# Performance work log

Measured on AMD Instinct MI355X. Metric: run time of the kernel, lower is better.

## Reference

```python
import jax, jax.numpy as jnp
import numpy as np

B, S, D, F, E = 2, 2048, 768, 3072, 8  # batch, seq, d_model, d_ff, n_experts


def setup_inputs() -> dict:
    key = jax.random.key(0)
    k0, k1, k2, k3 = jax.random.split(key, 4)
    return {
        "x": jax.random.normal(k0, (B, S, D), dtype=jnp.float32),
        "w_switch": jax.random.normal(k1, (D, E), dtype=jnp.float32) * 0.02,
        "b_switch": jnp.zeros((E,), dtype=jnp.float32),
        "wi": jax.random.normal(k2, (E, D, F), dtype=jnp.float32) * 0.02,
        "wo": jax.random.normal(k3, (E, F, D), dtype=jnp.float32) * 0.02,
    }


def reference(x, w_switch, b_switch, wi, wo):
    # SwitchFFN forward (drop_tokens=False, is_scale_prob=False, eval dropout).
    Bb, Ss, Dd = x.shape
    n_experts = wi.shape[0]
    xf = x.reshape(-1, Dd)                                # [T, D]
    route_prob = jax.nn.softmax(xf @ w_switch + b_switch, axis=-1)  # [T, E]
    route_prob_max = jnp.max(route_prob, axis=-1)         # [T]
    routes = jnp.argmax(route_prob, axis=-1)              # [T] int
    # factor = p_max / p_max.detach(): value 1, gradient flows through router
    factor = route_prob_max / jax.lax.stop_gradient(route_prob_max)
    xs = xf * factor[:, None]                             # [T, D]

    final_output = jnp.zeros_like(xf)
    for e in range(n_experts):                            # small fixed expert loop
        mask = (routes == e)[:, None]                     # [T, 1] bool
        xe = jnp.where(mask, xs, 0.0)                     # zero non-routed tokens
        ye = jax.nn.relu(xe @ wi[e]) @ wo[e]              # expert FFN [T, D]
        final_output = final_output + jnp.where(mask, ye, 0.0)

    counts = jnp.sum(jax.nn.one_hot(routes, n_experts, dtype=xf.dtype), axis=0)  # [E]
    route_prob_sum = jnp.sum(route_prob, axis=0)          # [E]
    n_dropped = jnp.array(0, dtype=jnp.int32)             # drop_tokens=False
    return final_output.reshape(Bb, Ss, Dd), counts, route_prob_sum, n_dropped
```

## Files before the change

kernel.cpp:

```cpp
#include <hip/hip_runtime.h>
#include <stdint.h>

#define T_TOK   4096
#define D_MODEL 768
#define F_FF    3072
#define N_EXP   8
#define BM      128
#define MAX_TILES 40
#define MCAP    (MAX_TILES * BM)

typedef __attribute__((ext_vector_type(4))) float  floatx4;
typedef __attribute__((ext_vector_type(8))) short  short8;

__device__ __forceinline__ unsigned short f2bf(float f) {
    union { float f; unsigned int u; } v; v.f = f;
    unsigned int u = v.u;
    unsigned int r = (u + 0x7FFFu + ((u >> 16) & 1u)) >> 16;
    return (unsigned short)r;
}
__device__ __forceinline__ float bf2f(unsigned short h) {
    union { unsigned int u; float f; } v; v.u = ((unsigned int)h) << 16;
    return v.f;
}

__global__ __launch_bounds__(256) void router_kernel(
        const float* __restrict__ x, const float* __restrict__ wsw,
        const float* __restrict__ bsw, int* __restrict__ routes,
        int* __restrict__ cnt_part, float* __restrict__ rps_part) {
    __shared__ float srps[N_EXP];
    __shared__ int   scnt[N_EXP];
    int tid = threadIdx.x;
    if (tid < N_EXP) { srps[tid] = 0.f; scnt[tid] = 0; }
    __syncthreads();
    int wave = tid >> 6, l = tid & 63;
    int t = blockIdx.x * 4 + wave;
    const float* xr = x + (size_t)t * D_MODEL;
    double acc[N_EXP];
#pragma unroll
    for (int e = 0; e < N_EXP; e++) acc[e] = 0.0;
    for (int d = l; d < D_MODEL; d += 64) {
        float xv = xr[d];
        const float* wr = wsw + d * N_EXP;
#pragma unroll
        for (int e = 0; e < N_EXP; e++) acc[e] += (double)xv * (double)wr[e];
    }
#pragma unroll
    for (int off = 32; off > 0; off >>= 1) {
#pragma unroll
        for (int e = 0; e < N_EXP; e++) acc[e] += __shfl_xor(acc[e], off, 64);
    }
    if (l == 0) {
        float logit[N_EXP];
        float mx = -1e30f; int am = 0;
#pragma unroll
        for (int e = 0; e < N_EXP; e++) {
            logit[e] = (float)acc[e] + bsw[e];
            if (logit[e] > mx) { mx = logit[e]; am = e; }
        }
        float p[N_EXP]; float s = 0.f;
#pragma unroll
        for (int e = 0; e < N_EXP; e++) { p[e] = __expf(logit[e] - mx); s += p[e]; }
        float inv = 1.f / s;
        routes[t] = am;
        atomicAdd(&scnt[am], 1);
#pragma unroll
        for (int e = 0; e < N_EXP; e++) atomicAdd(&srps[e], p[e] * inv);
    }
    __syncthreads();
    if (tid < N_EXP) {
        cnt_part[blockIdx.x * N_EXP + tid] = scnt[tid];
        rps_part[blockIdx.x * N_EXP + tid] = srps[tid];
    }
}

__global__ __launch_bounds__(256) void plan_kernel(
        const int* __restrict__ cnt_part, const float* __restrict__ rps_part,
        int* __restrict__ cnt, float* __restrict__ rps,
        int* __restrict__ astart, int* __restrict__ cursor,
        int* __restrict__ tile_e, int* __restrict__ tile_m0,
        float* __restrict__ out_tail) {
    __shared__ int   sc[N_EXP][32];
    __shared__ float sp[N_EXP][32];
    int tid = threadIdx.x;
    int e = tid & 7, chunk = tid >> 3;
    int ci = 0; float pf = 0.f;
#pragma unroll 4
    for (int b = chunk * 32; b < chunk * 32 + 32; b++) {
        ci += cnt_part[b * N_EXP + e];
        pf += rps_part[b * N_EXP + e];
    }
    sc[e][chunk] = ci; sp[e][chunk] = pf;
    __syncthreads();
    if (tid < N_EXP) {
        int s = 0; float f = 0.f;
        for (int c2 = 0; c2 < 32; c2++) { s += sc[tid][c2]; f += sp[tid][c2]; }
        cnt[tid] = s; rps[tid] = f;
        out_tail[tid] = (float)s;
        out_tail[N_EXP + tid] = f;
    }
    __syncthreads();
    if (tid == 0) {
        out_tail[2 * N_EXP] = 0.0f;
        int a = 0, idx = 0;
        for (int e2 = 0; e2 < N_EXP; e2++) {
            astart[e2] = a; cursor[e2] = a;
            int nt = (cnt[e2] + BM - 1) / BM;
            for (int j = 0; j < nt; j++) { tile_e[idx] = e2; tile_m0[idx] = a + j * BM; idx++; }
            a += nt * BM;
        }
        for (; idx < MAX_TILES; idx++) { tile_e[idx] = -1; tile_m0[idx] = 0; }
    }
}

__global__ __launch_bounds__(256) void assign_kernel(
        const int* __restrict__ routes, int* __restrict__ cursor,
        int* __restrict__ perm, int* __restrict__ tinv) {
    __shared__ int lcnt[N_EXP], sbase[N_EXP];
    int tid = threadIdx.x;
    if (tid < N_EXP) lcnt[tid] = 0;
    __syncthreads();
    int t = blockIdx.x * 256 + tid;
    int e = routes[t];
    int rank = atomicAdd(&lcnt[e], 1);
    __syncthreads();
    if (tid < N_EXP) sbase[tid] = atomicAdd(&cursor[tid], lcnt[tid]);
    __syncthreads();
    int pos = sbase[e] + rank;
    perm[pos] = t;
    tinv[t] = pos;
}

__global__ __launch_bounds__(256) void gather_kernel(
        const float* __restrict__ x, const int* __restrict__ tinv,
        unsigned short* __restrict__ Xs) {
    int wave = threadIdx.x >> 6, l = threadIdx.x & 63;
    int t = blockIdx.x * 4 + wave;
    int pos = tinv[t];
    const float4* src = (const float4*)(x + (size_t)t * D_MODEL);
    ushort4* dst = (ushort4*)(Xs + (size_t)pos * D_MODEL);
#pragma unroll
    for (int i = 0; i < 3; i++) {
        float4 v = src[i * 64 + l];
        ushort4 o;
        o.x = f2bf(v.x); o.y = f2bf(v.y); o.z = f2bf(v.z); o.w = f2bf(v.w);
        dst[i * 64 + l] = o;
    }
}

__global__ __launch_bounds__(256) void transpose_cast_kernel(
        const float* __restrict__ src, unsigned short* __restrict__ dst, int R, int C) {
    __shared__ float tile[64][65];
    int e = blockIdx.z;
    const float* s = src + (size_t)e * R * C;
    unsigned short* d = dst + (size_t)e * R * C;
    int tx = threadIdx.x & 63;
    int ty = threadIdx.x >> 6;
    int c0 = blockIdx.x * 64, r0 = blockIdx.y * 64;
#pragma unroll
    for (int k = 0; k < 16; k++) {
        int r = ty * 16 + k;
        tile[r][tx] = s[(size_t)(r0 + r) * C + (c0 + tx)];
    }
    __syncthreads();
    int rg = threadIdx.x & 15;
    int ch = threadIdx.x >> 4;
#pragma unroll
    for (int k = 0; k < 4; k++) {
        int c = ch + 16 * k;
        ushort4 v;
        v.x = f2bf(tile[4 * rg + 0][c]);
        v.y = f2bf(tile[4 * rg + 1][c]);
        v.z = f2bf(tile[4 * rg + 2][c]);
        v.w = f2bf(tile[4 * rg + 3][c]);
        *(ushort4*)(&d[(size_t)(c0 + c) * R + (r0 + 4 * rg)]) = v;
    }
}

#define GLL(gaddr, laddr) \
    __builtin_amdgcn_global_load_lds((const __attribute__((address_space(1))) unsigned int*)(gaddr), \
                                     (__attribute__((address_space(3))) unsigned int*)(laddr), 16, 0, 0)

__global__ __launch_bounds__(256) void gemm1_kernel(
        const unsigned short* __restrict__ A, const unsigned short* __restrict__ Bt,
        const int* __restrict__ tile_e, const int* __restrict__ tile_m0,
        unsigned short* __restrict__ Obf) {
    const int K = D_MODEL, N = F_FF;
    int e = tile_e[blockIdx.y];
    if (e < 0) return;
    int m0 = tile_m0[blockIdx.y];
    int n0 = blockIdx.x * 128;
    const unsigned short* Be = Bt + (size_t)e * N * K;

    __shared__ __align__(16) unsigned short ldsA[128 * 64];
    __shared__ __align__(16) unsigned short ldsB[128 * 64];

    int tid = threadIdx.x;
    int w = tid >> 6, l = tid & 63;
    int wm = w & 1, wn = w >> 1;
    int quad = l >> 4, l15 = l & 15;
    int s7 = l15 & 7;

    floatx4 zero = {0.f, 0.f, 0.f, 0.f};
    floatx4 acc[4][4];
#pragma unroll
    for (int i = 0; i < 4; i++)
#pragma unroll
        for (int j = 0; j < 4; j++) acc[i][j] = zero;

    int rl = l >> 3;
    int q  = (l & 7) ^ rl;
    int r0 = w * 8 + rl;
    const char* gA = (const char*)(A + (size_t)(m0 + r0) * K) + q * 16;
    const char* gB = (const char*)(Be + (size_t)(n0 + r0) * K) + q * 16;
    char* lA = (char*)ldsA + w * 1024;
    char* lB = (char*)ldsB + w * 1024;
    const size_t rowskip = (size_t)32 * K * 2;

#pragma unroll 1
    for (int kc = 0; kc < K; kc += 64) {
        const char* ga = gA + kc * 2;
        const char* gb = gB + kc * 2;
#pragma unroll
        for (int s = 0; s < 4; s++) {
            GLL(ga + s * rowskip, lA + s * 4096);
            GLL(gb + s * rowskip, lB + s * 4096);
        }
        __syncthreads();
#pragma unroll
        for (int kk = 0; kk < 2; kk++) {
            int p = (kk * 4 + quad) ^ s7;
            short8 af[4], bf[4];
#pragma unroll
            for (int i = 0; i < 4; i++)
                af[i] = *(const short8*)((const char*)ldsA + (wm * 64 + i * 16 + l15) * 128 + p * 16);
#pragma unroll
            for (int j = 0; j < 4; j++)
                bf[j] = *(const short8*)((const char*)ldsB + (wn * 64 + j * 16 + l15) * 128 + p * 16);
#pragma unroll
            for (int i = 0; i < 4; i++)
#pragma unroll
                for (int j = 0; j < 4; j++)
                    acc[i][j] = __builtin_amdgcn_mfma_f32_16x16x32_bf16(af[i], bf[j], acc[i][j], 0, 0, 0);
        }
        __syncthreads();
    }

#pragma unroll
    for (int i = 0; i < 4; i++) {
#pragma unroll
        for (int r = 0; r < 4; r++) {
            int row = m0 + wm * 64 + i * 16 + quad * 4 + r;
            size_t base = (size_t)row * N + n0 + wn * 64 + l15;
#pragma unroll
            for (int j = 0; j < 4; j++) {
                float v = acc[i][j][r];
                v = v > 0.f ? v : 0.f;
                Obf[base + j * 16] = f2bf(v);
            }
        }
    }
}

template <bool PARTIAL>
__global__ __launch_bounds__(256) void gemm2_kernel(
        const unsigned short* __restrict__ A, const unsigned short* __restrict__ Bt,
        const int* __restrict__ tile_e, const int* __restrict__ tile_m0,
        const int* __restrict__ perm, unsigned short* __restrict__ Pb,
        float* __restrict__ Of32) {
    const int K = F_FF, N = D_MODEL, KQ = F_FF / 4;
    int bid = blockIdx.x;
    int m_idx = bid % MAX_TILES;
    int strip = bid / MAX_TILES;
    int e = tile_e[m_idx];
    if (e < 0) return;
    int m0 = tile_m0[m_idx];
    int ks = strip / 6;
    int n0 = (strip % 6) * 128;
    const unsigned short* Be = Bt + (size_t)e * N * K;

    __shared__ __align__(16) unsigned short ldsA[128 * 64];
    __shared__ __align__(16) unsigned short ldsB[128 * 64];

    int tid = threadIdx.x;
    int w = tid >> 6, l = tid & 63;
    int wm = w & 1, wn = w >> 1;
    int quad = l >> 4, l15 = l & 15;
    int s7 = l15 & 7;

    floatx4 zero = {0.f, 0.f, 0.f, 0.f};
    floatx4 acc[4][4];
#pragma unroll
    for (int i = 0; i < 4; i++)
#pragma unroll
        for (int j = 0; j < 4; j++) acc[i][j] = zero;

    int rl = l >> 3;
    int q  = (l & 7) ^ rl;
    int r0 = w * 8 + rl;
    const char* gA = (const char*)(A + (size_t)(m0 + r0) * K) + q * 16;
    const char* gB = (const char*)(Be + (size_t)(n0 + r0) * K) + q * 16;
    char* lA = (char*)ldsA + w * 1024;
    char* lB = (char*)ldsB + w * 1024;
    const size_t rowskip = (size_t)32 * K * 2;

    int k_lo = ks * KQ, k_hi = k_lo + KQ;
#pragma unroll 1
    for (int kc = k_lo; kc < k_hi; kc += 64) {
        const char* ga = gA + kc * 2;
        const char* gb = gB + kc * 2;
#pragma unroll
        for (int s = 0; s < 4; s++) {
            GLL(ga + s * rowskip, lA + s * 4096);
            GLL(gb + s * rowskip, lB + s * 4096);
        }
        __syncthreads();
#pragma unroll
        for (int kk = 0; kk < 2; kk++) {
            int p = (kk * 4 + quad) ^ s7;
            short8 af[4], bf[4];
#pragma unroll
            for (int i = 0; i < 4; i++)
                af[i] = *(const short8*)((const char*)ldsA + (wm * 64 + i * 16 + l15) * 128 + p * 16);
#pragma unroll
            for (int j = 0; j < 4; j++)
                bf[j] = *(const short8*)((const char*)ldsB + (wn * 64 + j * 16 + l15) * 128 + p * 16);
#pragma unroll
            for (int i = 0; i < 4; i++)
#pragma unroll
                for (int j = 0; j < 4; j++)
                    acc[i][j] = __builtin_amdgcn_mfma_f32_16x16x32_bf16(af[i], bf[j], acc[i][j], 0, 0, 0);
        }
        __syncthreads();
    }

    if (PARTIAL) {
#pragma unroll
        for (int i = 0; i < 4; i++) {
#pragma unroll
            for (int r = 0; r < 4; r++) {
                int row = m0 + wm * 64 + i * 16 + quad * 4 + r;
                size_t base = (size_t)(ks * MCAP + row) * N + n0 + wn * 64 + l15;
#pragma unroll
                for (int j = 0; j < 4; j++)
                    Pb[base + j * 16] = f2bf(acc[i][j][r]);
            }
        }
    } else {
#pragma unroll
        for (int i = 0; i < 4; i++) {
#pragma unroll
            for (int r = 0; r < 4; r++) {
                int row = m0 + wm * 64 + i * 16 + quad * 4 + r;
                int t = perm[row];
                if (t < 0) continue;
                size_t base = (size_t)t * N + n0 + wn * 64 + l15;
#pragma unroll
                for (int j = 0; j < 4; j++)
                    atomicAdd(&Of32[base + j * 16], acc[i][j][r]);
            }
        }
    }
}

__global__ __launch_bounds__(256) void reduce_kernel(
        const unsigned short* __restrict__ Pb, const int* __restrict__ tinv,
        float* __restrict__ out) {
    int t = blockIdx.x;
    int m = tinv[t];
    const unsigned short* p0 = Pb + (size_t)m * D_MODEL;
    float* o = out + (size_t)t * D_MODEL;
#pragma unroll
    for (int it = 0; it < 3; it++) {
        int d = it * 256 + threadIdx.x;
        float s = 0.f;
#pragma unroll
        for (int ks = 0; ks < 4; ks++)
            s += bf2f(p0[(size_t)ks * MCAP * D_MODEL + d]);
        o[d] = s;
    }
}

extern "C" void kernel_launch(void* const* d_in, const int* in_sizes, int n_in,
                              void* d_out, int out_size, void* d_ws, size_t ws_size,
                              hipStream_t stream) {
    const float* x   = (const float*)d_in[0];
    const float* wsw = (const float*)d_in[1];
    const float* bsw = (const float*)d_in[2];
    const float* wi  = (const float*)d_in[3];
    const float* wo  = (const float*)d_in[4];
    float* out = (float*)d_out;

    char* ws = (char*)d_ws;
    int*   cnt      = (int*)(ws + 0);
    float* rps      = (float*)(ws + 32);
    int*   cursor   = (int*)(ws + 64);
    int*   astart   = (int*)(ws + 96);
    int*   tile_e   = (int*)(ws + 128);
    int*   tile_m0  = (int*)(ws + 288);
    int*   perm     = (int*)(ws + 512);
    int*   routes   = (int*)(ws + 20992);
    int*   tinv     = (int*)(ws + 37376);
    int*   cnt_part = (int*)(ws + 53760);
    float* rps_part = (float*)(ws + 86528);
    unsigned short* Xs = (unsigned short*)(ws + 119808);
    unsigned short* Y1 = (unsigned short*)(ws + 7984128);
    unsigned short* Wt = (unsigned short*)(ws + 39441408);
    unsigned short* Pb = (unsigned short*)(ws + 77190144);
    const bool use_partial = ws_size >= 108647424ull;

    hipMemsetAsync(ws + 512, 0xFF, MCAP * 4, stream);
    if (!use_partial)
        hipMemsetAsync(out, 0, (size_t)T_TOK * D_MODEL * 4, stream);

    router_kernel<<<T_TOK / 4, 256, 0, stream>>>(x, wsw, bsw, routes, cnt_part, rps_part);
    plan_kernel<<<1, 256, 0, stream>>>(cnt_part, rps_part, cnt, rps, astart, cursor,
                                       tile_e, tile_m0, out + (size_t)T_TOK * D_MODEL);
    assign_kernel<<<T_TOK / 256, 256, 0, stream>>>(routes, cursor, perm, tinv);
    gather_kernel<<<T_TOK / 4, 256, 0, stream>>>(x, tinv, Xs);

    transpose_cast_kernel<<<dim3(F_FF / 64, D_MODEL / 64, N_EXP), 256, 0, stream>>>(wi, Wt, D_MODEL, F_FF);
    gemm1_kernel<<<dim3(F_FF / 128, MAX_TILES), 256, 0, stream>>>(Xs, Wt, tile_e, tile_m0, Y1);

    transpose_cast_kernel<<<dim3(D_MODEL / 64, F_FF / 64, N_EXP), 256, 0, stream>>>(wo, Wt, F_FF, D_MODEL);
    if (use_partial) {
        gemm2_kernel<true><<<24 * MAX_TILES, 256, 0, stream>>>(Y1, Wt, tile_e, tile_m0, perm, Pb, out);
        reduce_kernel<<<T_TOK, 256, 0, stream>>>(Pb, tinv, out);
    } else {
        gemm2_kernel<false><<<24 * MAX_TILES, 256, 0, stream>>>(Y1, Wt, tile_e, tile_m0, perm, Pb, out);
    }
}
```

Measured before the change: 307.8 us.

## Double GEMM K-tile to 128, merge weight transposes into one launch, vectorize loads

```diff
diff --git a/kernel.cpp b/kernel.cpp
--- a/kernel.cpp
+++ b/kernel.cpp
@@ -148,22 +148,30 @@
 }
 
 __global__ __launch_bounds__(256) void transpose_cast_kernel(
-        const float* __restrict__ src, unsigned short* __restrict__ dst, int R, int C) {
-    __shared__ float tile[64][65];
-    int e = blockIdx.z;
-    const float* s = src + (size_t)e * R * C;
-    unsigned short* d = dst + (size_t)e * R * C;
-    int tx = threadIdx.x & 63;
-    int ty = threadIdx.x >> 6;
-    int c0 = blockIdx.x * 64, r0 = blockIdx.y * 64;
-#pragma unroll
-    for (int k = 0; k < 16; k++) {
-        int r = ty * 16 + k;
-        tile[r][tx] = s[(size_t)(r0 + r) * C + (c0 + tx)];
-    }
-    __syncthreads();
-    int rg = threadIdx.x & 15;
-    int ch = threadIdx.x >> 4;
+        const float* __restrict__ wi, const float* __restrict__ wo,
+        unsigned short* __restrict__ W1, unsigned short* __restrict__ W2, int zoff) {
+    __shared__ float tile[64][68];
+    int z = blockIdx.z + zoff;
+    const float* s; unsigned short* d; int R, C, bx, by;
+    if (z < 8) {
+        s = wi + (size_t)z * D_MODEL * F_FF; d = W1 + (size_t)z * D_MODEL * F_FF;
+        R = D_MODEL; C = F_FF; bx = blockIdx.x; by = blockIdx.y;
+    } else {
+        int e = z - 8;
+        s = wo + (size_t)e * F_FF * D_MODEL; d = W2 + (size_t)e * F_FF * D_MODEL;
+        R = F_FF; C = D_MODEL; bx = blockIdx.y; by = blockIdx.x;
+    }
+    int c0 = bx * 64, r0 = by * 64;
+    int rr = threadIdx.x >> 4, cg = threadIdx.x & 15;
+#pragma unroll
+    for (int k = 0; k < 4; k++) {
+        int r = rr + k * 16;
+        float4 v = *(const float4*)(s + (size_t)(r0 + r) * C + c0 + cg * 4);
+        tile[r][cg * 4 + 0] = v.x; tile[r][cg * 4 + 1] = v.y;
+        tile[r][cg * 4 + 2] = v.z; tile[r][cg * 4 + 3] = v.w;
+    }
+    __syncthreads();
+    int rg = threadIdx.x & 15, ch = threadIdx.x >> 4;
 #pragma unroll
     for (int k = 0; k < 4; k++) {
         int c = ch + 16 * k;
@@ -191,14 +199,13 @@
     int n0 = blockIdx.x * 128;
     const unsigned short* Be = Bt + (size_t)e * N * K;
 
-    __shared__ __align__(16) unsigned short ldsA[128 * 64];
-    __shared__ __align__(16) unsigned short ldsB[128 * 64];
+    __shared__ __align__(16) unsigned short ldsA[128 * 128];
+    __shared__ __align__(16) unsigned short ldsB[128 * 128];
 
     int tid = threadIdx.x;
     int w = tid >> 6, l = tid & 63;
     int wm = w & 1, wn = w >> 1;
     int quad = l >> 4, l15 = l & 15;
-    int s7 = l15 & 7;
 
     floatx4 zero = {0.f, 0.f, 0.f, 0.f};
     floatx4 acc[4][4];
@@ -207,35 +214,35 @@
 #pragma unroll
         for (int j = 0; j < 4; j++) acc[i][j] = zero;
 
-    int rl = l >> 3;
-    int q  = (l & 7) ^ rl;
-    int r0 = w * 8 + rl;
+    int rl = l >> 4;
+    int q  = (l & 15) ^ ((w * 4 + rl) & 15);
+    int r0 = w * 4 + rl;
     const char* gA = (const char*)(A + (size_t)(m0 + r0) * K) + q * 16;
     const char* gB = (const char*)(Be + (size_t)(n0 + r0) * K) + q * 16;
     char* lA = (char*)ldsA + w * 1024;
     char* lB = (char*)ldsB + w * 1024;
-    const size_t rowskip = (size_t)32 * K * 2;
+    const size_t rowskip = (size_t)16 * K * 2;
 
 #pragma unroll 1
-    for (int kc = 0; kc < K; kc += 64) {
+    for (int kc = 0; kc < K; kc += 128) {
         const char* ga = gA + kc * 2;
         const char* gb = gB + kc * 2;
 #pragma unroll
-        for (int s = 0; s < 4; s++) {
+        for (int s = 0; s < 8; s++) {
             GLL(ga + s * rowskip, lA + s * 4096);
             GLL(gb + s * rowskip, lB + s * 4096);
         }
         __syncthreads();
 #pragma unroll
-        for (int kk = 0; kk < 2; kk++) {
-            int p = (kk * 4 + quad) ^ s7;
+        for (int kk = 0; kk < 4; kk++) {
+            int p = (kk * 4 + quad) ^ l15;
             short8 af[4], bf[4];
 #pragma unroll
             for (int i = 0; i < 4; i++)
-                af[i] = *(const short8*)((const char*)ldsA + (wm * 64 + i * 16 + l15) * 128 + p * 16);
+                af[i] = *(const short8*)((const char*)ldsA + (wm * 64 + i * 16 + l15) * 256 + p * 16);
 #pragma unroll
             for (int j = 0; j < 4; j++)
-                bf[j] = *(const short8*)((const char*)ldsB + (wn * 64 + j * 16 + l15) * 128 + p * 16);
+                bf[j] = *(const short8*)((const char*)ldsB + (wn * 64 + j * 16 + l15) * 256 + p * 16);
 #pragma unroll
             for (int i = 0; i < 4; i++)
 #pragma unroll
@@ -278,14 +285,13 @@
     int n0 = (strip % 6) * 128;
     const unsigned short* Be = Bt + (size_t)e * N * K;
 
-    __shared__ __align__(16) unsigned short ldsA[128 * 64];
-    __shared__ __align__(16) unsigned short ldsB[128 * 64];
+    __shared__ __align__(16) unsigned short ldsA[128 * 128];
+    __shared__ __align__(16) unsigned short ldsB[128 * 128];
 
     int tid = threadIdx.x;
     int w = tid >> 6, l = tid & 63;
     int wm = w & 1, wn = w >> 1;
     int quad = l >> 4, l15 = l & 15;
-    int s7 = l15 & 7;
 
     floatx4 zero = {0.f, 0.f, 0.f, 0.f};
     floatx4 acc[4][4];
@@ -294,36 +300,36 @@
 #pragma unroll
         for (int j = 0; j < 4; j++) acc[i][j] = zero;
 
-    int rl = l >> 3;
-    int q  = (l & 7) ^ rl;
-    int r0 = w * 8 + rl;
+    int rl = l >> 4;
+    int q  = (l & 15) ^ ((w * 4 + rl) & 15);
+    int r0 = w * 4 + rl;
     const char* gA = (const char*)(A + (size_t)(m0 + r0) * K) + q * 16;
     const char* gB = (const char*)(Be + (size_t)(n0 + r0) * K) + q * 16;
     char* lA = (char*)ldsA + w * 1024;
     char* lB = (char*)ldsB + w * 1024;
-    const size_t rowskip = (size_t)32 * K * 2;
+    const size_t rowskip = (size_t)16 * K * 2;
 
     int k_lo = ks * KQ, k_hi = k_lo + KQ;
 #pragma unroll 1
-    for (int kc = k_lo; kc < k_hi; kc += 64) {
+    for (int kc = k_lo; kc < k_hi; kc += 128) {
         const char* ga = gA + kc * 2;
         const char* gb = gB + kc * 2;
 #pragma unroll
-        for (int s = 0; s < 4; s++) {
+        for (int s = 0; s < 8; s++) {
             GLL(ga + s * rowskip, lA + s * 4096);
             GLL(gb + s * rowskip, lB + s * 4096);
         }
         __syncthreads();
 #pragma unroll
-        for (int kk = 0; kk < 2; kk++) {
-            int p = (kk * 4 + quad) ^ s7;
+        for (int kk = 0; kk < 4; kk++) {
+            int p = (kk * 4 + quad) ^ l15;
             short8 af[4], bf[4];
 #pragma unroll
             for (int i = 0; i < 4; i++)
-                af[i] = *(const short8*)((const char*)ldsA + (wm * 64 + i * 16 + l15) * 128 + p * 16);
+                af[i] = *(const short8*)((const char*)ldsA + (wm * 64 + i * 16 + l15) * 256 + p * 16);
 #pragma unroll
             for (int j = 0; j < 4; j++)
-                bf[j] = *(const short8*)((const char*)ldsB + (wn * 64 + j * 16 + l15) * 128 + p * 16);
+                bf[j] = *(const short8*)((const char*)ldsB + (wn * 64 + j * 16 + l15) * 256 + p * 16);
 #pragma unroll
             for (int i = 0; i < 4; i++)
 #pragma unroll
@@ -402,15 +408,18 @@
     int*   tinv     = (int*)(ws + 37376);
     int*   cnt_part = (int*)(ws + 53760);
     float* rps_part = (float*)(ws + 86528);
-    unsigned short* Xs = (unsigned short*)(ws + 119808);
-    unsigned short* Y1 = (unsigned short*)(ws + 7984128);
-    unsigned short* Wt = (unsigned short*)(ws + 39441408);
-    unsigned short* Pb = (unsigned short*)(ws + 77190144);
+    unsigned short* Xs  = (unsigned short*)(ws + 119808);
+    unsigned short* Y1  = (unsigned short*)(ws + 7984128);
+    unsigned short* Wt1 = (unsigned short*)(ws + 39441408);
+    unsigned short* Pb  = (unsigned short*)(ws + 77190144);
+    unsigned short* Wt2 = (unsigned short*)(ws + 108647424);
     const bool use_partial = ws_size >= 108647424ull;
-
-    hipMemsetAsync(ws + 512, 0xFF, MCAP * 4, stream);
-    if (!use_partial)
+    const bool big_ws      = ws_size >= 146396160ull;
+
+    if (!use_partial) {
+        hipMemsetAsync(ws + 512, 0xFF, MCAP * 4, stream);
         hipMemsetAsync(out, 0, (size_t)T_TOK * D_MODEL * 4, stream);
+    }
 
     router_kernel<<<T_TOK / 4, 256, 0, stream>>>(x, wsw, bsw, routes, cnt_part, rps_part);
     plan_kernel<<<1, 256, 0, stream>>>(cnt_part, rps_part, cnt, rps, astart, cursor,
@@ -418,14 +427,20 @@
     assign_kernel<<<T_TOK / 256, 256, 0, stream>>>(routes, cursor, perm, tinv);
     gather_kernel<<<T_TOK / 4, 256, 0, stream>>>(x, tinv, Xs);
 
-    transpose_cast_kernel<<<dim3(F_FF / 64, D_MODEL / 64, N_EXP), 256, 0, stream>>>(wi, Wt, D_MODEL, F_FF);
-    gemm1_kernel<<<dim3(F_FF / 128, MAX_TILES), 256, 0, stream>>>(Xs, Wt, tile_e, tile_m0, Y1);
-
-    transpose_cast_kernel<<<dim3(D_MODEL / 64, F_FF / 64, N_EXP), 256, 0, stream>>>(wo, Wt, F_FF, D_MODEL);
-    if (use_partial) {
-        gemm2_kernel<true><<<24 * MAX_TILES, 256, 0, stream>>>(Y1, Wt, tile_e, tile_m0, perm, Pb, out);
+    if (big_ws) {
+        transpose_cast_kernel<<<dim3(F_FF / 64, D_MODEL / 64, 16), 256, 0, stream>>>(wi, wo, Wt1, Wt2, 0);
+        gemm1_kernel<<<dim3(F_FF / 128, MAX_TILES), 256, 0, stream>>>(Xs, Wt1, tile_e, tile_m0, Y1);
+        gemm2_kernel<true><<<24 * MAX_TILES, 256, 0, stream>>>(Y1, Wt2, tile_e, tile_m0, perm, Pb, out);
         reduce_kernel<<<T_TOK, 256, 0, stream>>>(Pb, tinv, out);
     } else {
-        gemm2_kernel<false><<<24 * MAX_TILES, 256, 0, stream>>>(Y1, Wt, tile_e, tile_m0, perm, Pb, out);
-    }
-}
+        transpose_cast_kernel<<<dim3(F_FF / 64, D_MODEL / 64, 8), 256, 0, stream>>>(wi, wo, Wt1, Wt1, 0);
+        gemm1_kernel<<<dim3(F_FF / 128, MAX_TILES), 256, 0, stream>>>(Xs, Wt1, tile_e, tile_m0, Y1);
+        transpose_cast_kernel<<<dim3(F_FF / 64, D_MODEL / 64, 8), 256, 0, stream>>>(wi, wo, Wt1, Wt1, 8);
+        if (use_partial) {
+            gemm2_kernel<true><<<24 * MAX_TILES, 256, 0, stream>>>(Y1, Wt1, tile_e, tile_m0, perm, Pb, out);
+            reduce_kernel<<<T_TOK, 256, 0, stream>>>(Pb, tinv, out);
+        } else {
+            gemm2_kernel<false><<<24 * MAX_TILES, 256, 0, stream>>>(Y1, Wt1, tile_e, tile_m0, perm, Pb, out);
+        }
+    }
+}
```

New measurement: 297.8 us. 3.2% less time.
